# Performance work log

Measured on AMD Instinct MI355X. Metric: run time of the kernel, lower is better.

## Reference

```python
import jax, jax.numpy as jnp
import numpy as np

NEG_INF = -9e15
ALPHA = 0.2  # LeakyReLU negative slope
OUT_FEATURES = 128


def setup_inputs() -> dict:
    key = jax.random.key(0)
    k1, k2, k3, k4 = jax.random.split(key, 4)
    B, N, F_in, F_out = 4, 4096, 256, OUT_FEATURES
    h = jax.random.normal(k1, (B, N, F_in), dtype=jnp.float32)
    adj = jax.random.randint(k2, (B, N, N), 0, 2, dtype=jnp.int32)
    W = jax.random.normal(k3, (F_in, F_out), dtype=jnp.float32) * 0.07
    a = jax.random.normal(k4, (2 * F_out, 1), dtype=jnp.float32) * 0.1
    return {"h": h, "adj": adj, "W": W, "a": a}


def reference(h, adj, W, a):
    # Wh: (B, N, F_out)
    Wh = jnp.einsum('bni,io->bno', h, W)
    a1 = a[:OUT_FEATURES, 0]   # (F_out,)
    a2 = a[OUT_FEATURES:, 0]   # (F_out,)
    Wh1 = Wh @ a1              # (B, N)
    Wh2 = Wh @ a2              # (B, N)
    e = Wh1[:, :, None] + Wh2[:, None, :]          # (B, N, N)
    e = jnp.where(e >= 0, e, ALPHA * e)             # LeakyReLU
    e = jnp.where(adj > 0, e, NEG_INF)              # adjacency mask
    attention = jax.nn.softmax(e, axis=-1)          # (B, N, N)
    # dropout omitted: reference runs in eval mode (training=False)
    h_prime = jnp.einsum('bnm,bmo->bno', attention, Wh)
    return jax.nn.elu(h_prime)  # concat=True
```

## Files before the change

### kernel.cpp

```cpp
#include <hip/hip_runtime.h>
#include <hip/hip_bf16.h>
#include <math.h>

typedef __attribute__((ext_vector_type(4))) float  f32x4;
typedef __attribute__((ext_vector_type(4))) int    i32x4;
typedef __attribute__((ext_vector_type(8))) short  s16x8;
typedef __attribute__((ext_vector_type(4))) short  s16x4;
typedef __attribute__((ext_vector_type(8))) __bf16 bf16x8;

#define LOG2E 1.4426950408889634f

__device__ __forceinline__ short f32_to_bf16_rne(float f) {
    unsigned u = __builtin_bit_cast(unsigned, f);
    u += 0x7fffu + ((u >> 16) & 1u);
    return (short)(u >> 16);
}
__device__ __forceinline__ bf16x8 as_bf16x8(s16x8 v) {
    return __builtin_bit_cast(bf16x8, v);
}

__global__ void k0_wt(const float* __restrict__ W, short* __restrict__ WT) {
    int g = blockIdx.x * 256 + threadIdx.x;
    int col = g >> 6;
    int k0 = (g & 63) * 4;
    s16x4 v;
    #pragma unroll
    for (int i = 0; i < 4; ++i) v[i] = f32_to_bf16_rne(W[(k0 + i) * 128 + col]);
    *(s16x4*)(WT + col * 256 + k0) = v;
}

__global__ __launch_bounds__(256, 2) void k1_gemm(
    const float* __restrict__ h, const float* __restrict__ a,
    const short* __restrict__ WT,
    short* __restrict__ WhT, float* __restrict__ Wh1p, float* __restrict__ Tp)
{
    int l = threadIdx.x & 63;
    int w = threadIdx.x >> 6;
    int gw = blockIdx.x * 4 + w;
    int r0 = gw * 16;
    int lm = l & 15, q = l >> 4;

    f32x4 acc[8];
    #pragma unroll
    for (int ct = 0; ct < 8; ++ct) acc[ct] = (f32x4)0.0f;

    const float* hrow = h + (long)(r0 + lm) * 256;
    for (int kb = 0; kb < 8; ++kb) {
        int kbase = kb * 32 + q * 8;
        f32x4 h0 = *(const f32x4*)(hrow + kbase);
        f32x4 h1 = *(const f32x4*)(hrow + kbase + 4);
        s16x8 af;
        #pragma unroll
        for (int j = 0; j < 4; ++j) af[j] = f32_to_bf16_rne(h0[j]);
        #pragma unroll
        for (int j = 0; j < 4; ++j) af[4 + j] = f32_to_bf16_rne(h1[j]);
        bf16x8 afb = as_bf16x8(af);
        #pragma unroll
        for (int ct = 0; ct < 8; ++ct) {
            s16x8 bf = *(const s16x8*)(WT + (ct * 16 + lm) * 256 + kbase);
            acc[ct] = __builtin_amdgcn_mfma_f32_16x16x32_bf16(afb, as_bf16x8(bf), acc[ct], 0, 0, 0);
        }
    }

    int b = r0 >> 12;
    int nb = r0 & 4095;
    float p1[4] = {0.f, 0.f, 0.f, 0.f}, p2[4] = {0.f, 0.f, 0.f, 0.f};
    #pragma unroll
    for (int ct = 0; ct < 8; ++ct) {
        int col = ct * 16 + lm;
        float a1c = a[col], a2c = a[128 + col];
        s16x4 vv;
        #pragma unroll
        for (int r = 0; r < 4; ++r) {
            float v = acc[ct][r];
            p1[r] += v * a1c;
            p2[r] += v * a2c;
            vv[r] = f32_to_bf16_rne(v);
        }
        *(s16x4*)(WhT + ((long)(b * 128 + col) * 4096 + nb + q * 4)) = vv;
    }
    #pragma unroll
    for (int off = 1; off < 16; off <<= 1) {
        #pragma unroll
        for (int r = 0; r < 4; ++r) {
            p1[r] += __shfl_xor(p1[r], off);
            p2[r] += __shfl_xor(p2[r], off);
        }
    }
    if (lm == 0) {
        #pragma unroll
        for (int r = 0; r < 4; ++r) {
            int row = r0 + q * 4 + r;
            Wh1p[row] = LOG2E * p1[r];
            Tp[row]   = LOG2E * p2[r];
        }
    }
}

__global__ void k2_tmax(const float* __restrict__ Tp, float* __restrict__ Tmax) {
    __shared__ float red[256];
    int b = blockIdx.x, t = threadIdx.x;
    float mx = -1e30f;
    for (int i = 0; i < 16; ++i) mx = fmaxf(mx, Tp[b * 4096 + t + i * 256]);
    red[t] = mx;
    __syncthreads();
    for (int s = 128; s > 0; s >>= 1) {
        if (t < s) red[t] = fmaxf(red[t], red[t + s]);
        __syncthreads();
    }
    if (t == 0) Tmax[b] = red[0];
}

template <int SPLIT, bool DIRECT>
__global__ __launch_bounds__(256, 2) void k3_attn(
    const int* __restrict__ adj, const short* __restrict__ WhT,
    const float* __restrict__ Wh1p, const float* __restrict__ Tp,
    const float* __restrict__ Tmax,
    float* __restrict__ U, float* __restrict__ Z, float* __restrict__ out)
{
    __shared__ __align__(16) short tile[128 * 128];
    int bid = blockIdx.x;
    int mh = bid % SPLIT;
    int nt = (bid / SPLIT) & 63;
    int b  = bid / (SPLIT * 64);
    int n0 = nt * 64;
    int l = threadIdx.x & 63, w = threadIdx.x >> 6;
    int lm = l & 15, q = l >> 4;

    int n_lane = n0 + w * 16 + lm;
    float sp  = Wh1p[b * 4096 + n_lane];
    float xm  = sp + Tmax[b];
    float Mrow = fmaxf(xm, 0.2f * xm);

    const int MTILES = 4096 / (SPLIT * 128);
    int mbase0 = mh * (4096 / SPLIT);

    const int*   adjrow = adj + ((long)(b * 4096 + n_lane) << 12);
    const float* tpb    = Tp + b * 4096;
    const short* whtb   = WhT + (long)b * 128 * 4096;

    f32x4 acc[8];
    #pragma unroll
    for (int ct = 0; ct < 8; ++ct) acc[ct] = (f32x4)0.0f;
    float z = 0.0f;

    #pragma unroll 1
    for (int ti = 0; ti < MTILES; ++ti) {
        int m0 = mbase0 + ti * 128;
        __syncthreads();
        {
            int colw = w * 32;
            #pragma unroll
            for (int j = 0; j < 8; ++j) {
                int cb = colw + j * 4;
                int col = cb + q;
                int gchunk = lm ^ (col & 7);
                const short* gp = whtb + (long)col * 4096 + m0 + gchunk * 8;
                short* lp = tile + cb * 128;
                __builtin_amdgcn_global_load_lds(
                    (const __attribute__((address_space(1))) void*)gp,
                    (__attribute__((address_space(3))) void*)lp,
                    16, 0, 0);
            }
        }
        i32x4 aj[8];
        f32x4 tv[8];
        #pragma unroll
        for (int ks = 0; ks < 4; ++ks) {
            int bm = m0 + ks * 32 + q * 8;
            aj[2 * ks]     = *(const i32x4*)(adjrow + bm);
            aj[2 * ks + 1] = *(const i32x4*)(adjrow + bm + 4);
            tv[2 * ks]     = *(const f32x4*)(tpb + bm);
            tv[2 * ks + 1] = *(const f32x4*)(tpb + bm + 4);
        }
        __syncthreads();

        #pragma unroll
        for (int ks = 0; ks < 4; ++ks) {
            s16x8 af;
            float zs = 0.0f;
            #pragma unroll
            for (int half = 0; half < 2; ++half) {
                i32x4 a4 = aj[2 * ks + half];
                f32x4 t4 = tv[2 * ks + half];
                #pragma unroll
                for (int j = 0; j < 4; ++j) {
                    float y = sp + t4[j];
                    float e = fmaxf(y, 0.2f * y) - Mrow;
                    float wv = exp2f(e);
                    wv = (a4[j] != 0) ? wv : 0.0f;
                    zs += wv;
                    af[half * 4 + j] = f32_to_bf16_rne(wv);
                }
            }
            z += zs;
            bf16x8 afb = as_bf16x8(af);
            #pragma unroll
            for (int ct = 0; ct < 8; ++ct) {
                int col = ct * 16 + lm;
                int pos = (ks * 4 + q) ^ (col & 7);
                s16x8 bf = *(const s16x8*)(tile + col * 128 + pos * 8);
                acc[ct] = __builtin_amdgcn_mfma_f32_16x16x32_bf16(afb, as_bf16x8(bf), acc[ct], 0, 0, 0);
            }
        }
    }

    z += __shfl_xor(z, 16);
    z += __shfl_xor(z, 32);

    if (DIRECT) {
        float zr[4];
        #pragma unroll
        for (int r = 0; r < 4; ++r) zr[r] = __shfl(z, q * 4 + r);
        float* orow = out + (long)(b * 4096 + n0 + w * 16) * 128;
        #pragma unroll
        for (int ct = 0; ct < 8; ++ct) {
            int col = ct * 16 + lm;
            #pragma unroll
            for (int r = 0; r < 4; ++r) {
                float x = acc[ct][r] / zr[r];
                orow[(q * 4 + r) * 128 + col] = (x > 0.f) ? x : (expf(x) - 1.0f);
            }
        }
    } else {
        if (l < 16) Z[(b * SPLIT + mh) * 4096 + n0 + w * 16 + lm] = z;
        float* ub = U + ((long)(b * SPLIT + mh) * 4096 + n0 + w * 16) * 128;
        #pragma unroll
        for (int ct = 0; ct < 8; ++ct) {
            int col = ct * 16 + lm;
            #pragma unroll
            for (int r = 0; r < 4; ++r)
                ub[(q * 4 + r) * 128 + col] = acc[ct][r];
        }
    }
}

__global__ void k4_combine(const float* __restrict__ U, const float* __restrict__ Z,
                           float* __restrict__ out) {
    long g = (long)blockIdx.x * 256 + threadIdx.x;
    long off = g * 4;
    long nf = off >> 7;
    int b = (int)(nf >> 12), n = (int)(nf & 4095), col = (int)(off & 127);
    long base0 = ((long)(b * 2) * 4096 + n) * 128 + col;
    f32x4 u0 = *(const f32x4*)(U + base0);
    f32x4 u1 = *(const f32x4*)(U + base0 + (long)4096 * 128);
    float zz = Z[(b * 2) * 4096 + n] + Z[(b * 2 + 1) * 4096 + n];
    f32x4 v;
    #pragma unroll
    for (int i = 0; i < 4; ++i) {
        float x = (u0[i] + u1[i]) / zz;
        v[i] = (x > 0.f) ? x : (expf(x) - 1.0f);
    }
    *(f32x4*)(out + off) = v;
}

extern "C" void kernel_launch(void* const* d_in, const int* in_sizes, int n_in,
                              void* d_out, int out_size, void* d_ws, size_t ws_size,
                              hipStream_t stream) {
    const float* h   = (const float*)d_in[0];
    const int*   adj = (const int*)d_in[1];
    const float* W   = (const float*)d_in[2];
    const float* a   = (const float*)d_in[3];
    float* out = (float*)d_out;

    char* ws = (char*)d_ws;
    short* WhT  = (short*)ws;
    short* WT   = (short*)(ws + 4194304);
    float* Wh1p = (float*)(ws + 4259840);
    float* Tp   = (float*)(ws + 4325376);
    float* Tmax = (float*)(ws + 4390912);
    float* U    = (float*)(ws + 4391168);
    float* Z    = (float*)(ws + 4391168 + 16777216);

    k0_wt<<<32, 256, 0, stream>>>(W, WT);
    k1_gemm<<<256, 256, 0, stream>>>(h, a, WT, WhT, Wh1p, Tp);
    k2_tmax<<<4, 256, 0, stream>>>(Tp, Tmax);

    bool split2 = ws_size >= (size_t)(4391168 + 16777216 + 131072);
    if (split2) {
        k3_attn<2, false><<<512, 256, 0, stream>>>(adj, WhT, Wh1p, Tp, Tmax, U, Z, out);
        k4_combine<<<2048, 256, 0, stream>>>(U, Z, out);
    } else {
        k3_attn<1, true><<<256, 256, 0, stream>>>(adj, WhT, Wh1p, Tp, Tmax, nullptr, nullptr, out);
    }
    (void)in_sizes; (void)n_in; (void)out_size;
}
```

Before: 421.4 us.

## Double-buffer WhT tiles and adjacency loads in attention kernel, cache Tp in LDS

```diff
diff --git a/kernel.cpp b/kernel.cpp
--- a/kernel.cpp
+++ b/kernel.cpp
@@ -15,7 +15,15 @@
     u += 0x7fffu + ((u >> 16) & 1u);
     return (short)(u >> 16);
 }
+__device__ __forceinline__ int pack2_bf16(float f0, float f1) {
+    unsigned u0 = __builtin_bit_cast(unsigned, f0) + 0x8000u;
+    unsigned u1 = __builtin_bit_cast(unsigned, f1) + 0x8000u;
+    return (int)((u0 >> 16) | (u1 & 0xffff0000u));
+}
 __device__ __forceinline__ bf16x8 as_bf16x8(s16x8 v) {
+    return __builtin_bit_cast(bf16x8, v);
+}
+__device__ __forceinline__ bf16x8 as_bf16x8(i32x4 v) {
     return __builtin_bit_cast(bf16x8, v);
 }
 
@@ -111,127 +119,136 @@
     if (t == 0) Tmax[b] = red[0];
 }
 
-template <int SPLIT, bool DIRECT>
+template <int SPLIT>
 __global__ __launch_bounds__(256, 2) void k3_attn(
     const int* __restrict__ adj, const short* __restrict__ WhT,
     const float* __restrict__ Wh1p, const float* __restrict__ Tp,
     const float* __restrict__ Tmax,
-    float* __restrict__ U, float* __restrict__ Z, float* __restrict__ out)
+    float* __restrict__ U, float* __restrict__ Z)
 {
-    __shared__ __align__(16) short tile[128 * 128];
-    int bid = blockIdx.x;
-    int mh = bid % SPLIT;
-    int nt = (bid / SPLIT) & 63;
-    int b  = bid / (SPLIT * 64);
-    int n0 = nt * 64;
+    const int MSLICE = 4096 / SPLIT;
+    const int MTILES = MSLICE / 128;
+    __shared__ __align__(16) short tile[2][128 * 128];
+    __shared__ __align__(16) float tps[4096 / SPLIT];
+
     int l = threadIdx.x & 63, w = threadIdx.x >> 6;
     int lm = l & 15, q = l >> 4;
+    int bid = blockIdx.x;
+    int mh = bid & (SPLIT - 1);
+    int rg = (bid / SPLIT) & 63;
+    int b  = bid / (SPLIT * 64);
+    int n0 = rg * 64;
+    int mbase = mh * MSLICE;
 
     int n_lane = n0 + w * 16 + lm;
-    float sp  = Wh1p[b * 4096 + n_lane];
-    float xm  = sp + Tmax[b];
+    float sp = Wh1p[b * 4096 + n_lane];
+    float xm = sp + Tmax[b];
     float Mrow = fmaxf(xm, 0.2f * xm);
 
-    const int MTILES = 4096 / (SPLIT * 128);
-    int mbase0 = mh * (4096 / SPLIT);
-
-    const int*   adjrow = adj + ((long)(b * 4096 + n_lane) << 12);
-    const float* tpb    = Tp + b * 4096;
+    const int*   adjrow = adj + ((long)(b * 4096 + n_lane) << 12) + q * 8;
     const short* whtb   = WhT + (long)b * 128 * 4096;
+    const float* tpsq   = tps + q * 8;
+
+    {
+        const float* tg = Tp + b * 4096 + mbase;
+        int i0 = threadIdx.x * 4;
+        *(f32x4*)(tps + i0)        = *(const f32x4*)(tg + i0);
+        *(f32x4*)(tps + i0 + 1024) = *(const f32x4*)(tg + i0 + 1024);
+    }
 
     f32x4 acc[8];
     #pragma unroll
     for (int ct = 0; ct < 8; ++ct) acc[ct] = (f32x4)0.0f;
     float z = 0.0f;
 
-    #pragma unroll 1
-    for (int ti = 0; ti < MTILES; ++ti) {
-        int m0 = mbase0 + ti * 128;
-        __syncthreads();
-        {
-            int colw = w * 32;
-            #pragma unroll
-            for (int j = 0; j < 8; ++j) {
-                int cb = colw + j * 4;
-                int col = cb + q;
-                int gchunk = lm ^ (col & 7);
-                const short* gp = whtb + (long)col * 4096 + m0 + gchunk * 8;
-                short* lp = tile + cb * 128;
-                __builtin_amdgcn_global_load_lds(
-                    (const __attribute__((address_space(1))) void*)gp,
-                    (__attribute__((address_space(3))) void*)lp,
-                    16, 0, 0);
-            }
-        }
-        i32x4 aj[8];
-        f32x4 tv[8];
+    auto stage = [&](short* dst, int m0) {
+        int colw = w * 32;
+        #pragma unroll
+        for (int j = 0; j < 8; ++j) {
+            int cb = colw + j * 4;
+            int col = cb + q;
+            int gch = lm ^ (col & 7);
+            const short* gp = whtb + (long)col * 4096 + m0 + gch * 8;
+            __builtin_amdgcn_global_load_lds(
+                (const __attribute__((address_space(1))) void*)gp,
+                (__attribute__((address_space(3))) void*)(dst + cb * 128), 16, 0, 0);
+        }
+    };
+    auto ldadj = [&](i32x4* aj, int m0) {
         #pragma unroll
         for (int ks = 0; ks < 4; ++ks) {
-            int bm = m0 + ks * 32 + q * 8;
-            aj[2 * ks]     = *(const i32x4*)(adjrow + bm);
-            aj[2 * ks + 1] = *(const i32x4*)(adjrow + bm + 4);
-            tv[2 * ks]     = *(const f32x4*)(tpb + bm);
-            tv[2 * ks + 1] = *(const f32x4*)(tpb + bm + 4);
-        }
-        __syncthreads();
-
+            aj[2 * ks]     = *(const i32x4*)(adjrow + m0 + ks * 32);
+            aj[2 * ks + 1] = *(const i32x4*)(adjrow + m0 + ks * 32 + 4);
+        }
+    };
+    auto compute = [&](const short* buf, const i32x4* aj, int mrel) {
         #pragma unroll
         for (int ks = 0; ks < 4; ++ks) {
-            s16x8 af;
+            f32x4 t0 = *(const f32x4*)(tpsq + mrel + ks * 32);
+            f32x4 t1 = *(const f32x4*)(tpsq + mrel + ks * 32 + 4);
+            i32x4 pk;
             float zs = 0.0f;
             #pragma unroll
             for (int half = 0; half < 2; ++half) {
                 i32x4 a4 = aj[2 * ks + half];
-                f32x4 t4 = tv[2 * ks + half];
+                f32x4 t4 = half ? t1 : t0;
+                float wv[4];
                 #pragma unroll
                 for (int j = 0; j < 4; ++j) {
                     float y = sp + t4[j];
                     float e = fmaxf(y, 0.2f * y) - Mrow;
-                    float wv = exp2f(e);
-                    wv = (a4[j] != 0) ? wv : 0.0f;
-                    zs += wv;
-                    af[half * 4 + j] = f32_to_bf16_rne(wv);
+                    float v = __builtin_amdgcn_exp2f(e);
+                    v = (a4[j] != 0) ? v : 0.0f;
+                    zs += v; wv[j] = v;
                 }
+                pk[half * 2]     = pack2_bf16(wv[0], wv[1]);
+                pk[half * 2 + 1] = pack2_bf16(wv[2], wv[3]);
             }
             z += zs;
-            bf16x8 afb = as_bf16x8(af);
+            bf16x8 ab = as_bf16x8(pk);
             #pragma unroll
             for (int ct = 0; ct < 8; ++ct) {
                 int col = ct * 16 + lm;
                 int pos = (ks * 4 + q) ^ (col & 7);
-                s16x8 bf = *(const s16x8*)(tile + col * 128 + pos * 8);
-                acc[ct] = __builtin_amdgcn_mfma_f32_16x16x32_bf16(afb, as_bf16x8(bf), acc[ct], 0, 0, 0);
+                s16x8 bf = *(const s16x8*)(buf + col * 128 + pos * 8);
+                acc[ct] = __builtin_amdgcn_mfma_f32_16x16x32_bf16(ab, as_bf16x8(bf), acc[ct], 0, 0, 0);
             }
         }
+    };
+
+    i32x4 ajA[8], ajB[8];
+    stage(tile[0], mbase);
+    ldadj(ajA, mbase);
+    __syncthreads();
+
+    #pragma unroll 1
+    for (int t = 0; t < MTILES; t += 2) {
+        int r1 = (t + 1) & (MTILES - 1);
+        stage(tile[1], mbase + r1 * 128);
+        ldadj(ajB, mbase + r1 * 128);
+        __builtin_amdgcn_sched_barrier(0);
+        compute(tile[0], ajA, t * 128);
+        __syncthreads();
+        int r2 = (t + 2) & (MTILES - 1);
+        stage(tile[0], mbase + r2 * 128);
+        ldadj(ajA, mbase + r2 * 128);
+        __builtin_amdgcn_sched_barrier(0);
+        compute(tile[1], ajB, r1 * 128);
+        __syncthreads();
     }
 
     z += __shfl_xor(z, 16);
     z += __shfl_xor(z, 32);
 
-    if (DIRECT) {
-        float zr[4];
-        #pragma unroll
-        for (int r = 0; r < 4; ++r) zr[r] = __shfl(z, q * 4 + r);
-        float* orow = out + (long)(b * 4096 + n0 + w * 16) * 128;
-        #pragma unroll
-        for (int ct = 0; ct < 8; ++ct) {
-            int col = ct * 16 + lm;
-            #pragma unroll
-            for (int r = 0; r < 4; ++r) {
-                float x = acc[ct][r] / zr[r];
-                orow[(q * 4 + r) * 128 + col] = (x > 0.f) ? x : (expf(x) - 1.0f);
-            }
-        }
-    } else {
-        if (l < 16) Z[(b * SPLIT + mh) * 4096 + n0 + w * 16 + lm] = z;
-        float* ub = U + ((long)(b * SPLIT + mh) * 4096 + n0 + w * 16) * 128;
-        #pragma unroll
-        for (int ct = 0; ct < 8; ++ct) {
-            int col = ct * 16 + lm;
-            #pragma unroll
-            for (int r = 0; r < 4; ++r)
-                ub[(q * 4 + r) * 128 + col] = acc[ct][r];
-        }
+    int slice = b * SPLIT + mh;
+    if (l < 16) Z[slice * 4096 + n0 + w * 16 + lm] = z;
+    float* ub = U + ((long)slice * 4096 + n0 + w * 16) * 128;
+    #pragma unroll
+    for (int ct = 0; ct < 8; ++ct) {
+        int col = ct * 16 + lm;
+        #pragma unroll
+        for (int r = 0; r < 4; ++r)
+            ub[(q * 4 + r) * 128 + col] = acc[ct][r];
     }
 }
 
@@ -275,13 +292,7 @@
     k0_wt<<<32, 256, 0, stream>>>(W, WT);
     k1_gemm<<<256, 256, 0, stream>>>(h, a, WT, WhT, Wh1p, Tp);
     k2_tmax<<<4, 256, 0, stream>>>(Tp, Tmax);
-
-    bool split2 = ws_size >= (size_t)(4391168 + 16777216 + 131072);
-    if (split2) {
-        k3_attn<2, false><<<512, 256, 0, stream>>>(adj, WhT, Wh1p, Tp, Tmax, U, Z, out);
-        k4_combine<<<2048, 256, 0, stream>>>(U, Z, out);
-    } else {
-        k3_attn<1, true><<<256, 256, 0, stream>>>(adj, WhT, Wh1p, Tp, Tmax, nullptr, nullptr, out);
-    }
-    (void)in_sizes; (void)n_in; (void)out_size;
-}
+    k3_attn<2><<<512, 256, 0, stream>>>(adj, WhT, Wh1p, Tp, Tmax, U, Z);
+    k4_combine<<<2048, 256, 0, stream>>>(U, Z, out);
+    (void)in_sizes; (void)n_in; (void)out_size; (void)ws_size;
+}
```

Result: faster. 404.7 us (-4.0%).
